# Performance work log

Hardware: AMD Instinct MI355X
Metric: run time of the kernel (lower is better)

Reference implementation:

```python
import jax, jax.numpy as jnp
import numpy as np

QMIN, QMAX = -128, 127  # 8-bit symmetric
EPS = 1e-8

def _fake_quant(v, scale, axis):
    # per-channel symmetric fake quant: round, clamp, dequant
    shape = [1] * v.ndim
    shape[axis] = -1
    s = (jnp.abs(scale) + EPS).reshape(shape)
    q = jnp.clip(jnp.round(v / s), QMIN, QMAX)
    return q * s

def setup_inputs() -> dict:
    key = jax.random.key(0)
    k1, k2, k3, k4, k5 = jax.random.split(key, 5)
    B, C_in, L = 32, 512, 4096
    C_out, K = 512, 3
    return {
        "x": jax.random.normal(k1, (B, C_in, L), dtype=jnp.float32),
        "weight": jax.random.normal(k2, (C_out, C_in, K), dtype=jnp.float32) * 0.05,
        "bias": jax.random.normal(k3, (C_out,), dtype=jnp.float32) * 0.1,
        "a_scale": jax.random.uniform(k4, (C_in,), dtype=jnp.float32, minval=0.01, maxval=0.1),
        "w_scale": jax.random.uniform(k5, (C_out,), dtype=jnp.float32, minval=0.001, maxval=0.01),
    }

def reference(x, weight, bias, a_scale, w_scale):
    # activations: per-channel (axis=1 of NCL) symmetric int8 fake-quant
    x_hat = _fake_quant(x, a_scale, axis=1)
    # weights: per-out-channel (axis=0 of OIK) symmetric int8 fake-quant
    w_hat = _fake_quant(weight, w_scale, axis=0)
    out = jax.lax.conv_general_dilated(
        x_hat, w_hat,
        window_strides=(1,), padding=[(1, 1)], rhs_dilation=(1,),
        dimension_numbers=("NCH", "OIH", "NCH"))
    return out + bias[None, :, None]
```

## Files before the change

### kernel.cpp

```cpp
#include <hip/hip_runtime.h>
#include <hip/hip_bf16.h>
#include <stdint.h>

#define BATCH 32
#define CIN   512
#define LLEN  4096
#define COUT  512
#define KW    3
#define KTOT  (CIN * KW)
#define LPAD  (LLEN + 2)
#define EPSQ  1e-8f

typedef __bf16 bf16x8 __attribute__((ext_vector_type(8)));
typedef float  floatx4 __attribute__((ext_vector_type(4)));

__device__ __forceinline__ void async_load16(const void* gptr, void* ldsptr) {
    __builtin_amdgcn_global_load_lds(
        (const __attribute__((address_space(1))) void*)gptr,
        (__attribute__((address_space(3))) void*)ldsptr,
        16, 0, 0);
}

__global__ void zero_pad_kernel(uint32_t* __restrict__ qxT_u32) {
    int idx = blockIdx.x * blockDim.x + threadIdx.x;
    int b = idx >> 9;
    int r = (idx >> 8) & 1;
    int c = idx & 255;
    size_t row = (size_t)b * LPAD + (r ? (LPAD - 1) : 0);
    qxT_u32[row * (CIN / 2) + c] = 0u;
}

__global__ __launch_bounds__(256) void quantx_kernel(
        const float* __restrict__ x,
        const float* __restrict__ a_scale,
        __bf16* __restrict__ qxT) {
    __shared__ __bf16 qs[64][66];
    const int i0 = blockIdx.x * 64;
    const int l0 = blockIdx.y * 64;
    const int b  = blockIdx.z;
    const int tid = threadIdx.x;
    const int r = tid >> 6;
    const int c = tid & 63;

    const float* xb = x + ((size_t)b * CIN + i0) * LLEN + l0;
    #pragma unroll
    for (int p = 0; p < 16; ++p) {
        int i = p * 4 + r;
        float s = fabsf(a_scale[i0 + i]) + EPSQ;
        float v = xb[(size_t)i * LLEN + c];
        float q = fminf(fmaxf(rintf(v / s), -128.0f), 127.0f);
        qs[c][i] = (__bf16)q;
    }
    __syncthreads();

    const int c2 = tid & 31;
    const int rr = tid >> 5;
    uint32_t* outp = (uint32_t*)(qxT + ((size_t)b * LPAD + (l0 + 1)) * CIN + i0);
    #pragma unroll
    for (int p = 0; p < 8; ++p) {
        int l = p * 8 + rr;
        union { __bf16 h[2]; uint32_t u; } pk;
        pk.h[0] = qs[l][2 * c2];
        pk.h[1] = qs[l][2 * c2 + 1];
        outp[(size_t)l * (CIN / 2) + c2] = pk.u;
    }
}

__global__ void wfold_kernel(
        const float* __restrict__ w,
        const float* __restrict__ a_scale,
        const float* __restrict__ w_scale,
        __bf16* __restrict__ Wf) {
    int idx = blockIdx.x * blockDim.x + threadIdx.x;
    if (idx >= COUT * KTOT) return;
    int o   = idx / KTOT;
    int rem = idx - o * KTOT;
    int k = rem >> 9;
    int i = rem & 511;
    float sw = fabsf(w_scale[o]) + EPSQ;
    float sa = fabsf(a_scale[i]) + EPSQ;
    float q = fminf(fmaxf(rintf(w[((size_t)o * CIN + i) * KW + k] / sw), -128.0f), 127.0f);
    Wf[idx] = (__bf16)(q * sa * sw);
}

__global__ __launch_bounds__(256) void qconv_gemm(
        const __bf16* __restrict__ Wf,
        const __bf16* __restrict__ qxT,
        const float* __restrict__ bias,
        float* __restrict__ out) {
    __shared__ __attribute__((aligned(16))) __bf16 Asmem[128 * 64];
    __shared__ __attribute__((aligned(16))) __bf16 Bsmem[128 * 64];

    const int tid  = threadIdx.x;
    const int m0   = blockIdx.x * 128;
    const int l0   = blockIdx.y * 128;
    const int b    = blockIdx.z;
    const int wave = tid >> 6;
    const int lane = tid & 63;
    const int wm = wave >> 1, wn = wave & 1;
    const int row16 = lane & 15;
    const int quad  = lane >> 4;

    floatx4 acc[4][4];
    #pragma unroll
    for (int i = 0; i < 4; ++i)
        #pragma unroll
        for (int j = 0; j < 4; ++j)
            acc[i][j] = (floatx4){0.f, 0.f, 0.f, 0.f};

    const __bf16* qxb = qxT + (size_t)b * LPAD * CIN;

    for (int t = 0; t < KTOT / 64; ++t) {
        const int kk0  = t * 64;
        const int kblk = kk0 >> 9;
        const int i0   = kk0 & 511;

        #pragma unroll
        for (int j = 0; j < 4; ++j) {
            int chunk = j * 256 + tid;
            int arow  = chunk >> 3;
            int acol  = (chunk & 7) * 8;
            async_load16(Wf + (size_t)(m0 + arow) * KTOT + kk0 + acol,
                         (char*)Asmem + chunk * 16);
        }
        #pragma unroll
        for (int j = 0; j < 4; ++j) {
            int chunk = j * 256 + tid;
            int brow  = chunk >> 3;
            int bcol  = (chunk & 7) * 8;
            async_load16(qxb + (size_t)(l0 + brow + kblk) * CIN + i0 + bcol,
                         (char*)Bsmem + chunk * 16);
        }
        __syncthreads();

        #pragma unroll
        for (int ks = 0; ks < 2; ++ks) {
            bf16x8 afrag[4], bfrag[4];
            #pragma unroll
            for (int mt = 0; mt < 4; ++mt) {
                int arow = wm * 64 + mt * 16 + row16;
                afrag[mt] = *(const bf16x8*)(Asmem + arow * 64 + ks * 32 + quad * 8);
            }
            #pragma unroll
            for (int nt = 0; nt < 4; ++nt) {
                int brow = wn * 64 + nt * 16 + row16;
                bfrag[nt] = *(const bf16x8*)(Bsmem + brow * 64 + ks * 32 + quad * 8);
            }
            #pragma unroll
            for (int mt = 0; mt < 4; ++mt)
                #pragma unroll
                for (int nt = 0; nt < 4; ++nt)
                    acc[mt][nt] = __builtin_amdgcn_mfma_f32_16x16x32_bf16(
                        afrag[mt], bfrag[nt], acc[mt][nt], 0, 0, 0);
        }
        __syncthreads();
    }

    float* outb = out + (size_t)b * COUT * LLEN;
    #pragma unroll
    for (int mt = 0; mt < 4; ++mt) {
        #pragma unroll
        for (int r = 0; r < 4; ++r) {
            int o = m0 + wm * 64 + mt * 16 + quad * 4 + r;
            float bv = bias[o];
            #pragma unroll
            for (int nt = 0; nt < 4; ++nt) {
                int l = l0 + wn * 64 + nt * 16 + row16;
                outb[(size_t)o * LLEN + l] = acc[mt][nt][r] + bv;
            }
        }
    }
}

extern "C" void kernel_launch(void* const* d_in, const int* in_sizes, int n_in,
                              void* d_out, int out_size, void* d_ws, size_t ws_size,
                              hipStream_t stream) {
    const float* x       = (const float*)d_in[0];
    const float* weight  = (const float*)d_in[1];
    const float* bias    = (const float*)d_in[2];
    const float* a_scale = (const float*)d_in[3];
    const float* w_scale = (const float*)d_in[4];
    float* out = (float*)d_out;

    __bf16* Wf  = (__bf16*)d_ws;
    __bf16* qxT = (__bf16*)((char*)d_ws + (size_t)COUT * KTOT * sizeof(__bf16));

    wfold_kernel<<<dim3((COUT * KTOT) / 256), dim3(256), 0, stream>>>(
        weight, a_scale, w_scale, Wf);
    zero_pad_kernel<<<dim3(64), dim3(256), 0, stream>>>((uint32_t*)qxT);
    quantx_kernel<<<dim3(CIN / 64, LLEN / 64, BATCH), dim3(256), 0, stream>>>(
        x, a_scale, qxT);
    qconv_gemm<<<dim3(COUT / 128, LLEN / 128, BATCH), dim3(256), 0, stream>>>(
        Wf, qxT, bias, out);
}
```

Before: 754.9 us.

## Swizzle GEMM LDS tiles with XOR and vectorize quantx loads/stores

```diff
diff --git a/kernel.cpp b/kernel.cpp
--- a/kernel.cpp
+++ b/kernel.cpp
@@ -39,30 +39,35 @@
     const int l0 = blockIdx.y * 64;
     const int b  = blockIdx.z;
     const int tid = threadIdx.x;
-    const int r = tid >> 6;
-    const int c = tid & 63;
-
-    const float* xb = x + ((size_t)b * CIN + i0) * LLEN + l0;
-    #pragma unroll
-    for (int p = 0; p < 16; ++p) {
-        int i = p * 4 + r;
+
+    const int f4   = tid & 15;
+    const int irow = tid >> 4;
+    #pragma unroll
+    for (int p = 0; p < 4; ++p) {
+        int i = p * 16 + irow;
         float s = fabsf(a_scale[i0 + i]) + EPSQ;
-        float v = xb[(size_t)i * LLEN + c];
-        float q = fminf(fmaxf(rintf(v / s), -128.0f), 127.0f);
-        qs[c][i] = (__bf16)q;
+        float inv = 1.0f / s;
+        const floatx4* xrow = (const floatx4*)(x + ((size_t)(b * CIN + i0 + i)) * LLEN + l0);
+        floatx4 v = xrow[f4];
+        #pragma unroll
+        for (int j = 0; j < 4; ++j) {
+            float q = fminf(fmaxf(rintf(v[j] * inv), -128.0f), 127.0f);
+            qs[f4 * 4 + j][i] = (__bf16)q;
+        }
     }
     __syncthreads();
 
-    const int c2 = tid & 31;
-    const int rr = tid >> 5;
-    uint32_t* outp = (uint32_t*)(qxT + ((size_t)b * LPAD + (l0 + 1)) * CIN + i0);
-    #pragma unroll
-    for (int p = 0; p < 8; ++p) {
-        int l = p * 8 + rr;
-        union { __bf16 h[2]; uint32_t u; } pk;
-        pk.h[0] = qs[l][2 * c2];
-        pk.h[1] = qs[l][2 * c2 + 1];
-        outp[(size_t)l * (CIN / 2) + c2] = pk.u;
+    const int c4 = tid & 15;
+    const int rr = tid >> 4;
+    uint2* outp = (uint2*)(qxT + ((size_t)b * LPAD + (l0 + 1)) * CIN + i0);
+    #pragma unroll
+    for (int p = 0; p < 4; ++p) {
+        int l = p * 16 + rr;
+        const uint32_t* qrow = (const uint32_t*)&qs[l][0];
+        uint2 u;
+        u.x = qrow[2 * c4];
+        u.y = qrow[2 * c4 + 1];
+        outp[(size_t)l * (CIN / 4) + c4] = u;
     }
 }
 
@@ -119,16 +124,16 @@
         for (int j = 0; j < 4; ++j) {
             int chunk = j * 256 + tid;
             int arow  = chunk >> 3;
-            int acol  = (chunk & 7) * 8;
-            async_load16(Wf + (size_t)(m0 + arow) * KTOT + kk0 + acol,
+            int gcol  = (chunk & 7) ^ (arow & 7);
+            async_load16(Wf + (size_t)(m0 + arow) * KTOT + kk0 + gcol * 8,
                          (char*)Asmem + chunk * 16);
         }
         #pragma unroll
         for (int j = 0; j < 4; ++j) {
             int chunk = j * 256 + tid;
             int brow  = chunk >> 3;
-            int bcol  = (chunk & 7) * 8;
-            async_load16(qxb + (size_t)(l0 + brow + kblk) * CIN + i0 + bcol,
+            int gcol  = (chunk & 7) ^ (brow & 7);
+            async_load16(qxb + (size_t)(l0 + brow + kblk) * CIN + i0 + gcol * 8,
                          (char*)Bsmem + chunk * 16);
         }
         __syncthreads();
@@ -139,12 +144,14 @@
             #pragma unroll
             for (int mt = 0; mt < 4; ++mt) {
                 int arow = wm * 64 + mt * 16 + row16;
-                afrag[mt] = *(const bf16x8*)(Asmem + arow * 64 + ks * 32 + quad * 8);
+                int js   = (ks * 4 + quad) ^ (arow & 7);
+                afrag[mt] = *(const bf16x8*)(Asmem + arow * 64 + js * 8);
             }
             #pragma unroll
             for (int nt = 0; nt < 4; ++nt) {
                 int brow = wn * 64 + nt * 16 + row16;
-                bfrag[nt] = *(const bf16x8*)(Bsmem + brow * 64 + ks * 32 + quad * 8);
+                int js   = (ks * 4 + quad) ^ (brow & 7);
+                bfrag[nt] = *(const bf16x8*)(Bsmem + brow * 64 + js * 8);
             }
             #pragma unroll
             for (int mt = 0; mt < 4; ++mt)
```

After: 719.3 us. 4.7% less time.
